# Kernel optimization log

Hardware: AMD Instinct MI355X
Metric: run time of the kernel (lower is better)

## Reference

```python
import jax, jax.numpy as jnp
import numpy as np

B, N, C, H, KH = 4, 4096, 1024, 16, 5
HD = C // H  # head dim = 64


def setup_inputs() -> dict:
    key = jax.random.key(0)
    ks = jax.random.split(key, 4)
    return {
        "x": jax.random.normal(ks[0], (B, N, C), jnp.float32),
        "qkv_w": jax.random.normal(ks[1], (3 * C, C), jnp.float32) * 0.02,
        "qkv_b": jnp.zeros((3 * C,), jnp.float32),
        "proj_w": jax.random.normal(ks[2], (C, C), jnp.float32) * 0.02,
        "proj_b": jnp.zeros((C,), jnp.float32),
        "pos_enc": jnp.zeros((1, C), jnp.float32),  # torch init: zeros
        "dwc_w": jax.random.normal(ks[3], (HD, 1, KH, KH), jnp.float32) * 0.05,
        "dwc_b": jnp.zeros((HD,), jnp.float32),
        "num_heads": H,
    }


def reference(x, qkv_w, qkv_b, proj_w, proj_b, pos_enc, dwc_w, dwc_b, num_heads):
    b, n, c = x.shape
    h = num_heads
    hd = c // h
    kh = dwc_w.shape[2]

    qkv = x @ qkv_w.T + qkv_b                     # (b, n, 3c)
    q, k, v = jnp.split(qkv, 3, axis=-1)          # each (b, n, c)
    k = k + pos_enc[:, :c]                        # broadcast (1, c)
    q = jax.nn.relu(q)
    k = jax.nn.relu(k)

    def to_heads(t):  # (b, n, c) -> (b*h, n, hd)
        return t.reshape(b, n, h, hd).transpose(0, 2, 1, 3).reshape(b * h, n, hd)

    q, k, v = to_heads(q), to_heads(k), to_heads(v)

    # linear attention in fp32 (inputs already fp32)
    z = 1.0 / (jnp.einsum('bic,bc->bi', q, k.sum(axis=1)) + 1e-6)   # (bh, n)
    kv = jnp.einsum('bjc,bjd->bcd', k, v)                           # (bh, hd, hd)
    out = jnp.einsum('bic,bcd->bid', q, kv) * z[:, :, None]         # (bh, n, hd)

    # depthwise 2D conv on v viewed as (bh, hd, n, 1), kernel (hd,1,kh,kh), pad kh//2
    fm = v.transpose(0, 2, 1)[..., None]                            # (bh, hd, n, 1)
    pad = kh // 2
    fm = jax.lax.conv_general_dilated(
        fm, dwc_w, window_strides=(1, 1),
        padding=((pad, pad), (pad, pad)),
        dimension_numbers=('NCHW', 'OIHW', 'NCHW'),
        feature_group_count=hd,
    ) + dwc_b[None, :, None, None]
    out = out + fm[..., 0].transpose(0, 2, 1)                       # (bh, n, hd)

    out = out.reshape(b, h, n, hd).transpose(0, 2, 1, 3).reshape(b, n, c)
    return out @ proj_w.T + proj_b
```

## Files before the change

kernel.cpp:

```cpp
#include <hip/hip_runtime.h>


#define BB   4
#define NN   4096
#define CDIM 1024
#define NH   16
#define HDIM 64
#define BH   64

typedef __attribute__((ext_vector_type(8))) short short8;
typedef __attribute__((ext_vector_type(4))) float f32x4;
typedef unsigned short u16;

__device__ __forceinline__ float b2f(short s) {
    union { unsigned u; float f; } c;
    c.u = ((unsigned)(unsigned short)s) << 16;
    return c.f;
}
__device__ __forceinline__ u16 f2b(float f) {
    unsigned u = __float_as_uint(f);
    return (u16)((u + 0x7fffu + ((u >> 16) & 1u)) >> 16);
}
__device__ __forceinline__ void gload16(const void* g, void* l) {
    __builtin_amdgcn_global_load_lds((const __attribute__((address_space(1))) void*)g,
                                     (__attribute__((address_space(3))) void*)l, 16, 0, 0);
}

__global__ __launch_bounds__(256) void k_fill_diag(float* __restrict__ out, int n, float val)
{
    int i = blockIdx.x * 256 + threadIdx.x;
    if (i < n) out[i] = val;
}

__global__ __launch_bounds__(256) void k_f32_to_bf16(const float* __restrict__ in,
                                                     u16* __restrict__ out, int n4)
{
    int i = blockIdx.x * 256 + threadIdx.x;
    if (i < n4) {
        float4 v = reinterpret_cast<const float4*>(in)[i];
        ushort4 o;
        o.x = f2b(v.x); o.y = f2b(v.y); o.z = f2b(v.z); o.w = f2b(v.w);
        reinterpret_cast<ushort4*>(out)[i] = o;
    }
}

#define GEMM256_8PH()                                                                    \
    const int t = threadIdx.x;                                                           \
    const int l = t & 63, w = t >> 6;                                                    \
    const int wr = w >> 2, wc = w & 3;                                                   \
    const int fr = l & 15;                                                               \
    const int physE  = ((l >> 4) ^ ((fr >> 1) & 3)) * 8;                                 \
    const int qa     = ((l & 3) ^ ((l >> 3) & 3)) * 8;                                   \
    const int aRow   = w * 16 + (l >> 2);                                                \
    const u16* gA0 = A  + (size_t)(brow + aRow) * 1024 + qa;                             \
    const u16* gB0 = Bw + (size_t)(bcol + aRow) * 1024 + qa;                             \
    char* ldsc = (char*)lds;                                                             \
    const int afBase = (wr * 128 + fr) * 32 + physE;                                     \
    const int bfBase = 16384 + (wc * 64 + fr) * 32 + physE;                              \
    f32x4 acc[8][4];                                                                     \
    _Pragma("unroll")                                                                    \
    for (int m = 0; m < 8; ++m)                                                          \
        _Pragma("unroll")                                                                \
        for (int n = 0; n < 4; ++n) acc[m][n] = (f32x4){0.f, 0.f, 0.f, 0.f};             \
    auto STG = [&](int kt, int kh, int isB) {                                            \
        const u16* g = (isB ? gB0 : gA0) + kt * 64 + kh * 32;                            \
        char* d = ldsc + (kt & 1) * 65536 + isB * 32768 + kh * 16384 + w * 1024 + l * 16;\
        gload16(g,          d);                                                          \
        gload16(g + 131072, d + 8192);                                                   \
    };                                                                                   \
    STG(0,0,0); STG(0,0,1); STG(0,1,0); STG(0,1,1); STG(1,0,0); STG(1,0,1);              \
    asm volatile("s_waitcnt vmcnt(4)" ::: "memory");                                     \
    __builtin_amdgcn_sched_barrier(0);                                                   \
    __builtin_amdgcn_s_barrier();                                                        \
    __builtin_amdgcn_sched_barrier(0);                                                   \
    _Pragma("unroll 1")                                                                  \
    for (int kt = 0; kt < 16; ++kt) {                                                    \
        const int B0 = (kt & 1) * 32768;                                                 \
        short8 af[4], bf[4];                                                             \
        _Pragma("unroll")                                                                \
        for (int m = 0; m < 4; ++m)                                                      \
            af[m] = *reinterpret_cast<const short8*>(&lds[B0 + afBase + m * 512]);       \
        _Pragma("unroll")                                                                \
        for (int n = 0; n < 4; ++n)                                                      \
            bf[n] = *reinterpret_cast<const short8*>(&lds[B0 + bfBase + n * 512]);       \
        if (kt + 1 < 16) STG(kt + 1, 1, 0);                                              \
        __builtin_amdgcn_sched_barrier(0);                                               \
        __builtin_amdgcn_s_barrier();                                                    \
        asm volatile("s_waitcnt lgkmcnt(0)" ::: "memory");                               \
        __builtin_amdgcn_sched_barrier(0);                                               \
        __builtin_amdgcn_s_setprio(1);                                                   \
        _Pragma("unroll")                                                                \
        for (int m = 0; m < 4; ++m)                                                      \
            _Pragma("unroll")                                                            \
            for (int n = 0; n < 4; ++n)                                                  \
                acc[m][n] = __builtin_amdgcn_mfma_f32_16x16x32_bf16(af[m], bf[n], acc[m][n], 0, 0, 0); \
        __builtin_amdgcn_s_setprio(0);                                                   \
        __builtin_amdgcn_sched_barrier(0);                                               \
        __builtin_amdgcn_s_barrier();                                                    \
        __builtin_amdgcn_sched_barrier(0);                                               \
        _Pragma("unroll")                                                                \
        for (int m = 0; m < 4; ++m)                                                      \
            af[m] = *reinterpret_cast<const short8*>(&lds[B0 + afBase + (m + 4) * 512]); \
        if (kt + 1 < 16) STG(kt + 1, 1, 1);                                              \
        __builtin_amdgcn_sched_barrier(0);                                               \
        __builtin_amdgcn_s_barrier();                                                    \
        asm volatile("s_waitcnt lgkmcnt(0)" ::: "memory");                               \
        __builtin_amdgcn_sched_barrier(0);                                               \
        __builtin_amdgcn_s_setprio(1);                                                   \
        _Pragma("unroll")                                                                \
        for (int m = 0; m < 4; ++m)                                                      \
            _Pragma("unroll")                                                            \
            for (int n = 0; n < 4; ++n)                                                  \
                acc[m + 4][n] = __builtin_amdgcn_mfma_f32_16x16x32_bf16(af[m], bf[n], acc[m + 4][n], 0, 0, 0); \
        __builtin_amdgcn_s_setprio(0);                                                   \
        __builtin_amdgcn_sched_barrier(0);                                               \
        __builtin_amdgcn_s_barrier();                                                    \
        __builtin_amdgcn_sched_barrier(0);                                               \
        _Pragma("unroll")                                                                \
        for (int m = 0; m < 4; ++m)                                                      \
            af[m] = *reinterpret_cast<const short8*>(&lds[B0 + 8192 + afBase + m * 512]);\
        _Pragma("unroll")                                                                \
        for (int n = 0; n < 4; ++n)                                                      \
            bf[n] = *reinterpret_cast<const short8*>(&lds[B0 + 8192 + bfBase + n * 512]);\
        if (kt + 2 < 16) STG(kt + 2, 0, 0);                                              \
        __builtin_amdgcn_sched_barrier(0);                                               \
        __builtin_amdgcn_s_barrier();                                                    \
        asm volatile("s_waitcnt lgkmcnt(0)" ::: "memory");                               \
        __builtin_amdgcn_sched_barrier(0);                                               \
        __builtin_amdgcn_s_setprio(1);                                                   \
        _Pragma("unroll")                                                                \
        for (int m = 0; m < 4; ++m)                                                      \
            _Pragma("unroll")                                                            \
            for (int n = 0; n < 4; ++n)                                                  \
                acc[m][n] = __builtin_amdgcn_mfma_f32_16x16x32_bf16(af[m], bf[n], acc[m][n], 0, 0, 0); \
        __builtin_amdgcn_s_setprio(0);                                                   \
        __builtin_amdgcn_sched_barrier(0);                                               \
        __builtin_amdgcn_s_barrier();                                                    \
        __builtin_amdgcn_sched_barrier(0);                                               \
        _Pragma("unroll")                                                                \
        for (int m = 0; m < 4; ++m)                                                      \
            af[m] = *reinterpret_cast<const short8*>(&lds[B0 + 8192 + afBase + (m + 4) * 512]); \
        if (kt + 2 < 16) STG(kt + 2, 0, 1);                                              \
        __builtin_amdgcn_sched_barrier(0);                                               \
        __builtin_amdgcn_s_barrier();                                                    \
        asm volatile("s_waitcnt lgkmcnt(0)" ::: "memory");                               \
        __builtin_amdgcn_sched_barrier(0);                                               \
        __builtin_amdgcn_s_setprio(1);                                                   \
        _Pragma("unroll")                                                                \
        for (int m = 0; m < 4; ++m)                                                      \
            _Pragma("unroll")                                                            \
            for (int n = 0; n < 4; ++n)                                                  \
                acc[m + 4][n] = __builtin_amdgcn_mfma_f32_16x16x32_bf16(af[m], bf[n], acc[m + 4][n], 0, 0, 0); \
        __builtin_amdgcn_s_setprio(0);                                                   \
        __builtin_amdgcn_sched_barrier(0);                                               \
        if (kt < 15) { asm volatile("s_waitcnt vmcnt(4)" ::: "memory"); }                \
        else         { asm volatile("s_waitcnt vmcnt(0)" ::: "memory"); }                \
        __builtin_amdgcn_sched_barrier(0);                                               \
        __builtin_amdgcn_s_barrier();                                                    \
        __builtin_amdgcn_sched_barrier(0);                                               \
    }

__global__ __launch_bounds__(512, 2) void k_gemm1_256(
    const u16* __restrict__ A,
    const u16* __restrict__ Bw,
    const float* __restrict__ bias, const float* __restrict__ pos_enc,
    u16* __restrict__ q, u16* __restrict__ ktg, u16* __restrict__ v, u16* __restrict__ vtg)
{
    __shared__ u16 lds[65536];
    const int lid = blockIdx.y * 12 + blockIdx.x;
    const int swz = (lid & 7) * 96 + (lid >> 3);
    const int bcol = (swz % 12) * 256;
    const int brow = (swz / 12) * 256;

    GEMM256_8PH()

    const int part = bcol >> 10;
    {
        const int row_l = wr * 128 + (l >> 4) * 4;
        const int col_l = wc * 64 + fr;
        #pragma unroll
        for (int n = 0; n < 4; ++n) {
            const int col = col_l + n * 16;
            const int gc = bcol + col;
            const int c = gc & 1023;
            float bv = bias[gc];
            if (part == 1) bv += pos_enc[c];
            const int cc = col >> 3, in = col & 7;
            #pragma unroll
            for (int m = 0; m < 8; ++m)
                #pragma unroll
                for (int j = 0; j < 4; ++j) {
                    const int row = row_l + m * 16 + j;
                    float val = acc[m][n][j] + bv;
                    if (part != 2) val = fmaxf(val, 0.f);
                    lds[row * 256 + ((cc ^ (row & 7)) << 3) + in] = f2b(val);
                }
        }
    }
    __syncthreads();
    const int b_ = brow >> 12, i0 = brow & 4095;
    if (part != 1) {
        u16* dst = (part == 0) ? q : v;
        #pragma unroll
        for (int it = 0; it < 16; ++it) {
            const int id = it * 512 + t;
            const int row = id >> 5, cc = id & 31;
            short8 val = *reinterpret_cast<const short8*>(&lds[row * 256 + ((cc ^ (row & 7)) << 3)]);
            const int c2 = (bcol + cc * 8) & 1023;
            const int h2 = c2 >> 6, d2 = c2 & 63;
            *reinterpret_cast<short8*>(
                &dst[((size_t)(b_ * NH + h2) * NN + i0 + row) * HDIM + d2]) = val;
        }
    }
    if (part != 0) {
        u16* dstT = (part == 1) ? ktg : vtg;
        #pragma unroll
        for (int it = 0; it < 16; ++it) {
            const int id = it * 512 + t;
            const int cl = id & 255, jc = id >> 8;
            short8 vv;
            #pragma unroll
            for (int rr = 0; rr < 8; ++rr)
                vv[rr] = (short)lds[(jc * 8 + rr) * 256 + (((cl >> 3) ^ rr) << 3) + (cl & 7)];
            const int c2 = (bcol + cl) & 1023;
            const int h2 = c2 >> 6, d2 = c2 & 63;
            *reinterpret_cast<short8*>(
                &dstT[((size_t)(b_ * NH + h2) * HDIM + d2) * NN + i0 + jc * 8]) = vv;
        }
    }
}

__global__ __launch_bounds__(512, 2) void k_gemm2_256(
    const u16* __restrict__ A, const u16* __restrict__ Bw,
    const float* __restrict__ bias, float* __restrict__ out)
{
    __shared__ u16 lds[65536];
    const int lid = blockIdx.y * 4 + blockIdx.x;
    const int swz = (lid & 7) * 32 + (lid >> 3);
    const int bcol = (swz % 4) * 256;
    const int brow = (swz / 4) * 256;

    GEMM256_8PH()

    const int col_base = bcol + wc * 64 + fr;
    const int row_base = brow + wr * 128 + (l >> 4) * 4;
    #pragma unroll
    for (int n = 0; n < 4; ++n) {
        const int gc = col_base + n * 16;
        const float bv = bias[gc];
        #pragma unroll
        for (int m = 0; m < 8; ++m)
            #pragma unroll
            for (int j = 0; j < 4; ++j) {
                const int gr = row_base + m * 16 + j;
                out[(size_t)gr * CDIM + gc] = acc[m][n][j] + bv;
            }
    }
}

__global__ __launch_bounds__(256) void k_kv_mfma(
    const u16* __restrict__ ktg, const u16* __restrict__ vtg,
    float* __restrict__ part)
{
    __shared__ float red[4][5120];
    const int t = threadIdx.x, l = t & 63, w = t >> 6;
    const int bh = blockIdx.x, ch = blockIdx.y;
    const u16* kb = ktg + (size_t)bh * HDIM * NN;
    const u16* vb = vtg + (size_t)bh * HDIM * NN;
    const int j0 = ch * 1024 + w * 256;
    const int fr = l & 15, kf = (l >> 4) * 8;

    f32x4 acc[5][4];
    #pragma unroll
    for (int m = 0; m < 5; ++m)
        #pragma unroll
        for (int n = 0; n < 4; ++n) acc[m][n] = (f32x4){0.f, 0.f, 0.f, 0.f};
    short8 ones;
    #pragma unroll
    for (int i = 0; i < 8; ++i) ones[i] = (short)0x3F80;

    for (int js = 0; js < 256; js += 32) {
        const int jb = j0 + js + kf;
        short8 a[4], b[4];
        #pragma unroll
        for (int m = 0; m < 4; ++m)
            a[m] = *reinterpret_cast<const short8*>(&vb[(size_t)(m * 16 + fr) * NN + jb]);
        #pragma unroll
        for (int n = 0; n < 4; ++n)
            b[n] = *reinterpret_cast<const short8*>(&kb[(size_t)(n * 16 + fr) * NN + jb]);
        #pragma unroll
        for (int m = 0; m < 4; ++m)
            #pragma unroll
            for (int n = 0; n < 4; ++n)
                acc[m][n] = __builtin_amdgcn_mfma_f32_16x16x32_bf16(a[m], b[n], acc[m][n], 0, 0, 0);
        #pragma unroll
        for (int n = 0; n < 4; ++n)
            acc[4][n] = __builtin_amdgcn_mfma_f32_16x16x32_bf16(ones, b[n], acc[4][n], 0, 0, 0);
    }
    #pragma unroll
    for (int m = 0; m < 5; ++m)
        #pragma unroll
        for (int n = 0; n < 4; ++n)
            #pragma unroll
            for (int j = 0; j < 4; ++j)
                red[w][(m * 16 + (l >> 4) * 4 + j) * 64 + fr + n * 16] = acc[m][n][j];
    __syncthreads();
    float* po = part + ((size_t)ch * BH + bh) * 5120;
    for (int i = t; i < 5120; i += 256)
        po[i] = red[0][i] + red[1][i] + red[2][i] + red[3][i];
}

__global__ __launch_bounds__(256) void k_kv_red(
    const float* __restrict__ part, u16* __restrict__ kvt)
{
    const int bh = blockIdx.x, t = threadIdx.x;
    u16* base = kvt + bh * 5120;
    for (int i = t; i < 5120; i += 256) {
        float s = part[(size_t)(0 * BH + bh) * 5120 + i]
                + part[(size_t)(1 * BH + bh) * 5120 + i]
                + part[(size_t)(2 * BH + bh) * 5120 + i]
                + part[(size_t)(3 * BH + bh) * 5120 + i];
        base[i] = f2b(s);
    }
}

__global__ __launch_bounds__(256) void k_attn_mfma(
    const u16* __restrict__ q, const u16* __restrict__ v,
    const u16* __restrict__ kvt,
    const float* __restrict__ dwc_w, const float* __restrict__ dwc_b,
    u16* __restrict__ out2)
{
    __shared__ u16 att[4][64 * 68];
    const int t = threadIdx.x;
    const int l = t & 63, w = t >> 6;
    const int bh = blockIdx.x;
    const int tb = blockIdx.y * 256 + w * 64;
    const size_t hb = (size_t)bh * NN * HDIM;
    const u16* qb  = q + hb + (size_t)tb * HDIM;
    const u16* kvb = kvt + bh * 5120;

    const int fr = l & 15;
    const int kfrag = (l >> 4) * 8;

    short8 bfr[5][2];
    #pragma unroll
    for (int n = 0; n < 5; ++n)
        #pragma unroll
        for (int ks = 0; ks < 2; ++ks)
            bfr[n][ks] = *reinterpret_cast<const short8*>(&kvb[(n * 16 + fr) * 64 + ks * 32 + kfrag]);

    f32x4 acc[4][5];
    #pragma unroll
    for (int m = 0; m < 4; ++m)
        #pragma unroll
        for (int n = 0; n < 5; ++n) acc[m][n] = (f32x4){0.f, 0.f, 0.f, 0.f};

    #pragma unroll
    for (int m = 0; m < 4; ++m)
        #pragma unroll
        for (int ks = 0; ks < 2; ++ks) {
            short8 a = *reinterpret_cast<const short8*>(&qb[(m * 16 + fr) * 64 + ks * 32 + kfrag]);
            #pragma unroll
            for (int n = 0; n < 5; ++n)
                acc[m][n] = __builtin_amdgcn_mfma_f32_16x16x32_bf16(a, bfr[n][ks], acc[m][n], 0, 0, 0);
        }

    #pragma unroll
    for (int m = 0; m < 4; ++m)
        #pragma unroll
        for (int j = 0; j < 4; ++j) {
            const float den = __shfl(acc[m][4][j], l & 48);
            const float z = 1.f / (den + 1e-6f);
            const int row = m * 16 + (l >> 4) * 4 + j;
            #pragma unroll
            for (int n = 0; n < 4; ++n)
                att[w][row * 68 + fr + n * 16] = f2b(acc[m][n][j] * z);
        }
    __syncthreads();

    const int d = l;
    float w5[5];
    #pragma unroll
    for (int dh = 0; dh < 5; ++dh) w5[dh] = dwc_w[d * 25 + dh * 5 + 2];
    const float cbias = dwc_b[d];
    const int b_ = bh >> 4, h_ = bh & 15;
    u16* obase = out2 + (size_t)b_ * NN * CDIM + (size_t)h_ * 64 + d;
    float win[5];
    #pragma unroll
    for (int p = 0; p < 4; ++p) {
        const int src = tb - 2 + p;
        win[p] = (src >= 0 && src < NN) ? b2f(v[hb + (size_t)src * 64 + d]) : 0.f;
    }
    for (int it = 0; it < 64; ++it) {
        const int srcn = tb + it + 2;
        win[4] = (srcn < NN) ? b2f(v[hb + (size_t)srcn * 64 + d]) : 0.f;
        const float fm = cbias + w5[0] * win[0] + w5[1] * win[1] + w5[2] * win[2]
                               + w5[3] * win[3] + w5[4] * win[4];
        const float attn = b2f((short)att[w][it * 68 + d]);
        obase[(size_t)(tb + it) * CDIM] = f2b(attn + fm);
        win[0] = win[1]; win[1] = win[2]; win[2] = win[3]; win[3] = win[4];
    }
}

extern "C" void kernel_launch(void* const* d_in, const int* in_sizes, int n_in,
                              void* d_out, int out_size, void* d_ws, size_t ws_size,
                              hipStream_t stream)
{
    const float* x       = (const float*)d_in[0];
    const float* qkv_w   = (const float*)d_in[1];
    const float* qkv_b   = (const float*)d_in[2];
    const float* proj_w  = (const float*)d_in[3];
    const float* proj_b  = (const float*)d_in[4];
    const float* pos_enc = (const float*)d_in[5];
    const float* dwc_w   = (const float*)d_in[6];
    const float* dwc_b   = (const float*)d_in[7];

    const size_t QKV = 16777216;
    char* p = (char*)d_ws;
    u16* q_b    = (u16*)p;               p += QKV * 2;
    u16* ktg    = (u16*)p;               p += QKV * 2;
    u16* v_b    = (u16*)p;               p += QKV * 2;
    u16* vtg    = (u16*)p;               p += QKV * 2;
    u16* x_b    = (u16*)p;               p += QKV * 2;
    u16* qkvw_b = (u16*)p;               p += (size_t)3145728 * 2;
    u16* projw_b= (u16*)p;               p += (size_t)1048576 * 2;
    float* part = (float*)p;             p += (size_t)4 * BH * 5120 * 4;
    u16* kvt    = (u16*)p;               p += (size_t)(BH * 5120) * 2;
    const size_t need_bytes = (size_t)(p - (char*)d_ws);

    if (ws_size < need_bytes) {
        const float diag = 4096.0f + (float)(ws_size >> 20);
        k_fill_diag<<<(out_size + 255) / 256, 256, 0, stream>>>((float*)d_out, out_size, diag);
        return;
    }

    u16* out2 = ktg;
    float* out = (float*)d_out;

    k_f32_to_bf16<<<16384, 256, 0, stream>>>(x,      x_b,     4194304);
    k_f32_to_bf16<<< 3072, 256, 0, stream>>>(qkv_w,  qkvw_b,   786432);
    k_f32_to_bf16<<< 1024, 256, 0, stream>>>(proj_w, projw_b,  262144);

    k_gemm1_256 <<<dim3(12, 64), 512, 0, stream>>>(x_b, qkvw_b, qkv_b, pos_enc, q_b, ktg, v_b, vtg);
    k_kv_mfma   <<<dim3(64, 4),  256, 0, stream>>>(ktg, vtg, part);
    k_kv_red    <<<64,           256, 0, stream>>>(part, kvt);
    k_attn_mfma <<<dim3(64, 16), 256, 0, stream>>>(q_b, v_b, kvt, dwc_w, dwc_b, out2);
    k_gemm2_256 <<<dim3(4, 64),  512, 0, stream>>>(out2, projw_b, proj_b, out);
}
```

Measured before the change: 286.1 us.

## Merge conversion launches, drop row-major V copy, stage GEMM2 output via LDS

The three fp32-to-bf16 conversion kernels become one launch that picks its source buffer by index range. GEMM1 no longer writes a row-major copy of V, and the depthwise conv in the attention kernel now reads the transposed V buffer along contiguous rows. GEMM2's epilogue stages fp32 results through swizzled LDS in two halves so it can issue coalesced float4 stores instead of scattered scalar ones. These changes cut launch overhead and global write traffic, at the cost of extra barriers and LDS traffic in the GEMM2 epilogue. The conv's per-lane reads along separate transposed rows may also coalesce less well.

```diff
diff --git a/kernel.cpp b/kernel.cpp
--- a/kernel.cpp
+++ b/kernel.cpp
@@ -32,16 +32,19 @@
     if (i < n) out[i] = val;
 }
 
-__global__ __launch_bounds__(256) void k_f32_to_bf16(const float* __restrict__ in,
-                                                     u16* __restrict__ out, int n4)
+__global__ __launch_bounds__(256) void k_convert_all(
+    const float* __restrict__ x, const float* __restrict__ qw, const float* __restrict__ pw,
+    u16* __restrict__ xb, u16* __restrict__ qwb, u16* __restrict__ pwb)
 {
     int i = blockIdx.x * 256 + threadIdx.x;
-    if (i < n4) {
-        float4 v = reinterpret_cast<const float4*>(in)[i];
-        ushort4 o;
-        o.x = f2b(v.x); o.y = f2b(v.y); o.z = f2b(v.z); o.w = f2b(v.w);
-        reinterpret_cast<ushort4*>(out)[i] = o;
-    }
+    const float* src; u16* dst; int j;
+    if (i < 4194304)      { src = x;  dst = xb;  j = i; }
+    else if (i < 4980736) { src = qw; dst = qwb; j = i - 4194304; }
+    else                  { src = pw; dst = pwb; j = i - 4980736; }
+    float4 v = reinterpret_cast<const float4*>(src)[j];
+    ushort4 o;
+    o.x = f2b(v.x); o.y = f2b(v.y); o.z = f2b(v.z); o.w = f2b(v.w);
+    reinterpret_cast<ushort4*>(dst)[j] = o;
 }
 
 #define GEMM256_8PH()                                                                    \
@@ -161,10 +164,9 @@
     }
 
 __global__ __launch_bounds__(512, 2) void k_gemm1_256(
-    const u16* __restrict__ A,
-    const u16* __restrict__ Bw,
+    const u16* __restrict__ A, const u16* __restrict__ Bw,
     const float* __restrict__ bias, const float* __restrict__ pos_enc,
-    u16* __restrict__ q, u16* __restrict__ ktg, u16* __restrict__ v, u16* __restrict__ vtg)
+    u16* __restrict__ q, u16* __restrict__ ktg, u16* __restrict__ vtg)
 {
     __shared__ u16 lds[65536];
     const int lid = blockIdx.y * 12 + blockIdx.x;
@@ -199,8 +201,7 @@
     }
     __syncthreads();
     const int b_ = brow >> 12, i0 = brow & 4095;
-    if (part != 1) {
-        u16* dst = (part == 0) ? q : v;
+    if (part == 0) {
         #pragma unroll
         for (int it = 0; it < 16; ++it) {
             const int id = it * 512 + t;
@@ -209,10 +210,9 @@
             const int c2 = (bcol + cc * 8) & 1023;
             const int h2 = c2 >> 6, d2 = c2 & 63;
             *reinterpret_cast<short8*>(
-                &dst[((size_t)(b_ * NH + h2) * NN + i0 + row) * HDIM + d2]) = val;
-        }
-    }
-    if (part != 0) {
+                &q[((size_t)(b_ * NH + h2) * NN + i0 + row) * HDIM + d2]) = val;
+        }
+    } else {
         u16* dstT = (part == 1) ? ktg : vtg;
         #pragma unroll
         for (int it = 0; it < 16; ++it) {
@@ -242,19 +242,36 @@
 
     GEMM256_8PH()
 
-    const int col_base = bcol + wc * 64 + fr;
-    const int row_base = brow + wr * 128 + (l >> 4) * 4;
-    #pragma unroll
-    for (int n = 0; n < 4; ++n) {
-        const int gc = col_base + n * 16;
-        const float bv = bias[gc];
-        #pragma unroll
-        for (int m = 0; m < 8; ++m)
-            #pragma unroll
-            for (int j = 0; j < 4; ++j) {
-                const int gr = row_base + m * 16 + j;
-                out[(size_t)gr * CDIM + gc] = acc[m][n][j] + bv;
+    float* ldsf = reinterpret_cast<float*>(lds);
+    #pragma unroll 1
+    for (int half = 0; half < 2; ++half) {
+        __syncthreads();
+        if (wr == half) {
+            const int row_l = (l >> 4) * 4;
+            const int col_l = wc * 64 + fr;
+            #pragma unroll
+            for (int n = 0; n < 4; ++n) {
+                const int col = col_l + n * 16;
+                const float bv = bias[bcol + col];
+                #pragma unroll
+                for (int m = 0; m < 8; ++m)
+                    #pragma unroll
+                    for (int j = 0; j < 4; ++j) {
+                        const int row = m * 16 + row_l + j;
+                        ldsf[row * 256 + (col ^ (((row >> 2) & 3) << 3))] = acc[m][n][j] + bv;
+                    }
             }
+        }
+        __syncthreads();
+        const float4* ldsf4 = reinterpret_cast<const float4*>(ldsf);
+        #pragma unroll
+        for (int it = 0; it < 16; ++it) {
+            const int id = it * 512 + t;
+            const int row = id >> 6, cc4 = id & 63;
+            float4 vv = ldsf4[row * 64 + (cc4 ^ (((row >> 2) & 3) << 1))];
+            *reinterpret_cast<float4*>(
+                &out[(size_t)(brow + half * 128 + row) * CDIM + bcol + cc4 * 4]) = vv;
+        }
     }
 }
 
@@ -325,7 +342,7 @@
 }
 
 __global__ __launch_bounds__(256) void k_attn_mfma(
-    const u16* __restrict__ q, const u16* __restrict__ v,
+    const u16* __restrict__ q, const u16* __restrict__ vtg,
     const u16* __restrict__ kvt,
     const float* __restrict__ dwc_w, const float* __restrict__ dwc_b,
     u16* __restrict__ out2)
@@ -335,8 +352,7 @@
     const int l = t & 63, w = t >> 6;
     const int bh = blockIdx.x;
     const int tb = blockIdx.y * 256 + w * 64;
-    const size_t hb = (size_t)bh * NN * HDIM;
-    const u16* qb  = q + hb + (size_t)tb * HDIM;
+    const u16* qb  = q + (size_t)bh * NN * HDIM + (size_t)tb * HDIM;
     const u16* kvb = kvt + bh * 5120;
 
     const int fr = l & 15;
@@ -379,6 +395,7 @@
     __syncthreads();
 
     const int d = l;
+    const u16* vrow = vtg + (size_t)bh * HDIM * NN + (size_t)d * NN;
     float w5[5];
     #pragma unroll
     for (int dh = 0; dh < 5; ++dh) w5[dh] = dwc_w[d * 25 + dh * 5 + 2];
@@ -389,11 +406,11 @@
     #pragma unroll
     for (int p = 0; p < 4; ++p) {
         const int src = tb - 2 + p;
-        win[p] = (src >= 0 && src < NN) ? b2f(v[hb + (size_t)src * 64 + d]) : 0.f;
+        win[p] = (src >= 0 && src < NN) ? b2f(vrow[src]) : 0.f;
     }
     for (int it = 0; it < 64; ++it) {
         const int srcn = tb + it + 2;
-        win[4] = (srcn < NN) ? b2f(v[hb + (size_t)srcn * 64 + d]) : 0.f;
+        win[4] = (srcn < NN) ? b2f(vrow[srcn]) : 0.f;
         const float fm = cbias + w5[0] * win[0] + w5[1] * win[1] + w5[2] * win[2]
                                + w5[3] * win[3] + w5[4] * win[4];
         const float attn = b2f((short)att[w][it * 68 + d]);
@@ -419,7 +436,6 @@
     char* p = (char*)d_ws;
     u16* q_b    = (u16*)p;               p += QKV * 2;
     u16* ktg    = (u16*)p;               p += QKV * 2;
-    u16* v_b    = (u16*)p;               p += QKV * 2;
     u16* vtg    = (u16*)p;               p += QKV * 2;
     u16* x_b    = (u16*)p;               p += QKV * 2;
     u16* qkvw_b = (u16*)p;               p += (size_t)3145728 * 2;
@@ -437,13 +453,11 @@
     u16* out2 = ktg;
     float* out = (float*)d_out;
 
-    k_f32_to_bf16<<<16384, 256, 0, stream>>>(x,      x_b,     4194304);
-    k_f32_to_bf16<<< 3072, 256, 0, stream>>>(qkv_w,  qkvw_b,   786432);
-    k_f32_to_bf16<<< 1024, 256, 0, stream>>>(proj_w, projw_b,  262144);
-
-    k_gemm1_256 <<<dim3(12, 64), 512, 0, stream>>>(x_b, qkvw_b, qkv_b, pos_enc, q_b, ktg, v_b, vtg);
+    k_convert_all<<<20480, 256, 0, stream>>>(x, qkv_w, proj_w, x_b, qkvw_b, projw_b);
+
+    k_gemm1_256 <<<dim3(12, 64), 512, 0, stream>>>(x_b, qkvw_b, qkv_b, pos_enc, q_b, ktg, vtg);
     k_kv_mfma   <<<dim3(64, 4),  256, 0, stream>>>(ktg, vtg, part);
     k_kv_red    <<<64,           256, 0, stream>>>(part, kvt);
-    k_attn_mfma <<<dim3(64, 16), 256, 0, stream>>>(q_b, v_b, kvt, dwc_w, dwc_b, out2);
+    k_attn_mfma <<<dim3(64, 16), 256, 0, stream>>>(q_b, vtg, kvt, dwc_w, dwc_b, out2);
     k_gemm2_256 <<<dim3(4, 64),  512, 0, stream>>>(out2, projw_b, proj_b, out);
 }
```

Result: slower. 305.4 us (+6.7%).
